# Kernel optimization log

Measured on AMD Instinct MI355X. Metric: run time of the kernel, lower is better.

Reference implementation:

```python
import jax, jax.numpy as jnp
import numpy as np

N, D, E = 100000, 128, 1000000


def setup_inputs() -> dict:
    key = jax.random.key(0)
    k1, k2, k3 = jax.random.split(key, 3)
    index = jax.random.randint(k1, (E,), 0, N, dtype=jnp.int64 if jax.config.read('jax_enable_x64') else jnp.int32)
    A = jax.random.normal(k2, (N, D), dtype=jnp.float32)
    B = jax.random.normal(k3, (E, D), dtype=jnp.float32)
    return {"index": index, "A": A, "B": B}


def reference(index, A, B):
    # Sequential A[i] += B[count] with duplicate indices == scatter-add
    # (addition is commutative/associative, so one fused scatter suffices).
    return A.at[index].add(B)
```

## Files before the change

kernel.cpp:

```cpp
#include <hip/hip_runtime.h>

#define NROWS 100000
#define DDIM  128
#define ECNT  1000000

#define BUCK 64

__global__ void zero_counts(int* __restrict__ counts) {
    int i = blockIdx.x * blockDim.x + threadIdx.x;
    if (i < NROWS) counts[i] = 0;
}

__global__ void scatter_bucket(const int* __restrict__ index,
                               int* __restrict__ counts,
                               int* __restrict__ bucket) {
    int t  = blockIdx.x * blockDim.x + threadIdx.x;
    int e0 = t << 2;
    if (e0 >= ECNT) return;
    int4 r4 = *reinterpret_cast<const int4*>(index + e0);
    int p;
    p = atomicAdd(&counts[r4.x], 1); if (p < BUCK) bucket[r4.x * BUCK + p] = e0;
    p = atomicAdd(&counts[r4.y], 1); if (p < BUCK) bucket[r4.y * BUCK + p] = e0 + 1;
    p = atomicAdd(&counts[r4.z], 1); if (p < BUCK) bucket[r4.z * BUCK + p] = e0 + 2;
    p = atomicAdd(&counts[r4.w], 1); if (p < BUCK) bucket[r4.w * BUCK + p] = e0 + 3;
}

__global__ void gather_rows(const float* __restrict__ A, const float* __restrict__ B,
                            const int* __restrict__ bucket, const int* __restrict__ counts,
                            float* __restrict__ out) {
    int wave = (blockIdx.x * blockDim.x + threadIdx.x) >> 6;
    int lane = threadIdx.x & 63;
    if (wave >= NROWS) return;

    int cnt = counts[wave];
    if (cnt > BUCK) cnt = BUCK;

    int myperm = bucket[wave * BUCK + lane];

    const float2* Arow = (const float2*)(A + (size_t)wave * DDIM);
    float2 acc = Arow[lane];

    int j = 0;
    for (; j + 4 <= cnt; j += 4) {
        int e0 = __shfl(myperm, j + 0);
        int e1 = __shfl(myperm, j + 1);
        int e2 = __shfl(myperm, j + 2);
        int e3 = __shfl(myperm, j + 3);
        float2 b0 = ((const float2*)(B + (size_t)e0 * DDIM))[lane];
        float2 b1 = ((const float2*)(B + (size_t)e1 * DDIM))[lane];
        float2 b2 = ((const float2*)(B + (size_t)e2 * DDIM))[lane];
        float2 b3 = ((const float2*)(B + (size_t)e3 * DDIM))[lane];
        acc.x += b0.x; acc.y += b0.y;
        acc.x += b1.x; acc.y += b1.y;
        acc.x += b2.x; acc.y += b2.y;
        acc.x += b3.x; acc.y += b3.y;
    }
    for (; j < cnt; ++j) {
        int e = __shfl(myperm, j);
        float2 b = ((const float2*)(B + (size_t)e * DDIM))[lane];
        acc.x += b.x; acc.y += b.y;
    }

    float2* Orow = (float2*)(out + (size_t)wave * DDIM);
    Orow[lane] = acc;
}

extern "C" void kernel_launch(void* const* d_in, const int* in_sizes, int n_in,
                              void* d_out, int out_size, void* d_ws, size_t ws_size,
                              hipStream_t stream) {
    const int*   index = (const int*)d_in[0];
    const float* A     = (const float*)d_in[1];
    const float* B     = (const float*)d_in[2];
    float*       out   = (float*)d_out;

    int* counts = (int*)d_ws;
    int* bucket = counts + NROWS;

    zero_counts  <<<(NROWS + 255) / 256, 256, 0, stream>>>(counts);
    scatter_bucket<<<(ECNT / 4 + 255) / 256, 256, 0, stream>>>(index, counts, bucket);

    long long gthreads = (long long)NROWS * 64;
    int gblocks = (int)((gthreads + 255) / 256);
    gather_rows  <<<gblocks, 256, 0, stream>>>(A, B, bucket, counts, out);
}
```

Measured before the change: 790.3 us.

## Split wave into half-waves loading float4 rows with nontemporal B loads

The gather kernel now has each half of a wavefront process alternate bucket entries using 16-byte float4 loads with nontemporal hints, then combines the two halves with a cross-lane xor shuffle before a single half writes the row. The scatter kernel handles eight indices per thread and the zero kernel writes int4, which cuts thread counts. The goal is wider memory transactions and more B rows in flight per wave, at the cost of an extra reduction step and some divergence in the tail loop.

```diff
diff --git a/kernel.cpp b/kernel.cpp
--- a/kernel.cpp
+++ b/kernel.cpp
@@ -6,23 +6,32 @@
 
 #define BUCK 64
 
+typedef float f4v __attribute__((ext_vector_type(4)));
+
 __global__ void zero_counts(int* __restrict__ counts) {
     int i = blockIdx.x * blockDim.x + threadIdx.x;
-    if (i < NROWS) counts[i] = 0;
+    if (i < NROWS / 4) {
+        reinterpret_cast<int4*>(counts)[i] = make_int4(0, 0, 0, 0);
+    }
 }
 
 __global__ void scatter_bucket(const int* __restrict__ index,
                                int* __restrict__ counts,
                                int* __restrict__ bucket) {
     int t  = blockIdx.x * blockDim.x + threadIdx.x;
-    int e0 = t << 2;
+    int e0 = t << 3;
     if (e0 >= ECNT) return;
-    int4 r4 = *reinterpret_cast<const int4*>(index + e0);
+    int4 ra = *reinterpret_cast<const int4*>(index + e0);
+    int4 rb = *reinterpret_cast<const int4*>(index + e0 + 4);
     int p;
-    p = atomicAdd(&counts[r4.x], 1); if (p < BUCK) bucket[r4.x * BUCK + p] = e0;
-    p = atomicAdd(&counts[r4.y], 1); if (p < BUCK) bucket[r4.y * BUCK + p] = e0 + 1;
-    p = atomicAdd(&counts[r4.z], 1); if (p < BUCK) bucket[r4.z * BUCK + p] = e0 + 2;
-    p = atomicAdd(&counts[r4.w], 1); if (p < BUCK) bucket[r4.w * BUCK + p] = e0 + 3;
+    p = atomicAdd(&counts[ra.x], 1); if (p < BUCK) bucket[ra.x * BUCK + p] = e0;
+    p = atomicAdd(&counts[ra.y], 1); if (p < BUCK) bucket[ra.y * BUCK + p] = e0 + 1;
+    p = atomicAdd(&counts[ra.z], 1); if (p < BUCK) bucket[ra.z * BUCK + p] = e0 + 2;
+    p = atomicAdd(&counts[ra.w], 1); if (p < BUCK) bucket[ra.w * BUCK + p] = e0 + 3;
+    p = atomicAdd(&counts[rb.x], 1); if (p < BUCK) bucket[rb.x * BUCK + p] = e0 + 4;
+    p = atomicAdd(&counts[rb.y], 1); if (p < BUCK) bucket[rb.y * BUCK + p] = e0 + 5;
+    p = atomicAdd(&counts[rb.z], 1); if (p < BUCK) bucket[rb.z * BUCK + p] = e0 + 6;
+    p = atomicAdd(&counts[rb.w], 1); if (p < BUCK) bucket[rb.w * BUCK + p] = e0 + 7;
 }
 
 __global__ void gather_rows(const float* __restrict__ A, const float* __restrict__ B,
@@ -31,38 +40,51 @@
     int wave = (blockIdx.x * blockDim.x + threadIdx.x) >> 6;
     int lane = threadIdx.x & 63;
     if (wave >= NROWS) return;
+    int half = lane >> 5;
+    int col  = lane & 31;
 
     int cnt = counts[wave];
     if (cnt > BUCK) cnt = BUCK;
 
     int myperm = bucket[wave * BUCK + lane];
 
-    const float2* Arow = (const float2*)(A + (size_t)wave * DDIM);
-    float2 acc = Arow[lane];
+    const f4v* Arow = (const f4v*)(A + (size_t)wave * DDIM);
+    f4v a = Arow[col];
+    f4v acc = half ? (f4v)(0.0f) : a;
 
     int j = 0;
-    for (; j + 4 <= cnt; j += 4) {
-        int e0 = __shfl(myperm, j + 0);
-        int e1 = __shfl(myperm, j + 1);
-        int e2 = __shfl(myperm, j + 2);
-        int e3 = __shfl(myperm, j + 3);
-        float2 b0 = ((const float2*)(B + (size_t)e0 * DDIM))[lane];
-        float2 b1 = ((const float2*)(B + (size_t)e1 * DDIM))[lane];
-        float2 b2 = ((const float2*)(B + (size_t)e2 * DDIM))[lane];
-        float2 b3 = ((const float2*)(B + (size_t)e3 * DDIM))[lane];
-        acc.x += b0.x; acc.y += b0.y;
-        acc.x += b1.x; acc.y += b1.y;
-        acc.x += b2.x; acc.y += b2.y;
-        acc.x += b3.x; acc.y += b3.y;
+    for (; j + 8 <= cnt; j += 8) {
+        int e0 = __shfl(myperm, j     + half);
+        int e1 = __shfl(myperm, j + 2 + half);
+        int e2 = __shfl(myperm, j + 4 + half);
+        int e3 = __shfl(myperm, j + 6 + half);
+        f4v b0 = __builtin_nontemporal_load((const f4v*)(B + (size_t)e0 * DDIM) + col);
+        f4v b1 = __builtin_nontemporal_load((const f4v*)(B + (size_t)e1 * DDIM) + col);
+        f4v b2 = __builtin_nontemporal_load((const f4v*)(B + (size_t)e2 * DDIM) + col);
+        f4v b3 = __builtin_nontemporal_load((const f4v*)(B + (size_t)e3 * DDIM) + col);
+        acc += b0; acc += b1; acc += b2; acc += b3;
     }
-    for (; j < cnt; ++j) {
-        int e = __shfl(myperm, j);
-        float2 b = ((const float2*)(B + (size_t)e * DDIM))[lane];
-        acc.x += b.x; acc.y += b.y;
+    for (; j < cnt; j += 2) {
+        int idx = j + half;
+        bool valid = idx < cnt;
+        int e = __shfl(myperm, valid ? idx : 0);
+        if (valid) {
+            f4v b = __builtin_nontemporal_load((const f4v*)(B + (size_t)e * DDIM) + col);
+            acc += b;
+        }
     }
 
-    float2* Orow = (float2*)(out + (size_t)wave * DDIM);
-    Orow[lane] = acc;
+    f4v other;
+    other.x = __shfl_xor(acc.x, 32);
+    other.y = __shfl_xor(acc.y, 32);
+    other.z = __shfl_xor(acc.z, 32);
+    other.w = __shfl_xor(acc.w, 32);
+    acc += other;
+
+    if (half == 0) {
+        f4v* Orow = (f4v*)(out + (size_t)wave * DDIM);
+        Orow[col] = acc;
+    }
 }
 
 extern "C" void kernel_launch(void* const* d_in, const int* in_sizes, int n_in,
@@ -76,10 +98,10 @@
     int* counts = (int*)d_ws;
     int* bucket = counts + NROWS;
 
-    zero_counts  <<<(NROWS + 255) / 256, 256, 0, stream>>>(counts);
-    scatter_bucket<<<(ECNT / 4 + 255) / 256, 256, 0, stream>>>(index, counts, bucket);
+    zero_counts   <<<(NROWS / 4 + 255) / 256, 256, 0, stream>>>(counts);
+    scatter_bucket<<<(ECNT / 8 + 255) / 256, 256, 0, stream>>>(index, counts, bucket);
 
     long long gthreads = (long long)NROWS * 64;
     int gblocks = (int)((gthreads + 255) / 256);
-    gather_rows  <<<gblocks, 256, 0, stream>>>(A, B, bucket, counts, out);
+    gather_rows   <<<gblocks, 256, 0, stream>>>(A, B, bucket, counts, out);
 }
```

After: 763.0 us. 1.04x faster.
